# Kernel tuning notes

Measured on AMD Instinct MI355X. Metric: run time of the kernel, lower is better.

## Reference

```python
import jax, jax.numpy as jnp
import numpy as np
import math

JULIA_ITERS = 64
ESCAPE_RADIUS = 2.0


def _julia_escape_times(seq_len, c_real, c_imag):
    # Positions mapped to the real segment [-2, 2]; iterate z <- z^2 + c,
    # record (first iteration index where |z| > R) / ITERS, else 1.0.
    x = jnp.linspace(-2.0, 2.0, seq_len)
    zr0 = x
    zi0 = jnp.zeros_like(x)
    escaped0 = jnp.zeros(seq_len, dtype=bool)
    et0 = jnp.ones(seq_len, dtype=x.dtype)
    r2 = ESCAPE_RADIUS * ESCAPE_RADIUS

    def step(carry, it):
        zr, zi, escaped, et = carry
        nzr = zr * zr - zi * zi + c_real
        nzi = 2.0 * zr * zi + c_imag
        # torch breaks out of the loop once escaped -> freeze z afterwards
        zr = jnp.where(escaped, zr, nzr)
        zi = jnp.where(escaped, zi, nzi)
        mag2 = zr * zr + zi * zi
        newly = jnp.logical_and(~escaped, mag2 > r2)
        et = jnp.where(newly, it.astype(et.dtype) / JULIA_ITERS, et)
        escaped = jnp.logical_or(escaped, newly)
        return (zr, zi, escaped, et), None

    (_, _, _, et), _ = jax.lax.scan(step, (zr0, zi0, escaped0, et0), jnp.arange(JULIA_ITERS))
    return et


def setup_inputs() -> dict:
    key = jax.random.key(0)
    kq, kk, kv = jax.random.split(key, 3)
    B, S, D = 4, 8192, 64
    return {
        "query": jax.random.normal(kq, (B, S, D), dtype=jnp.float32),
        "key": jax.random.normal(kk, (B, S, D), dtype=jnp.float32),
        "value": jax.random.normal(kv, (B, S, D), dtype=jnp.float32),
        "julia_c_real": jnp.float32(-0.7),
        "julia_c_imag": jnp.float32(0.27),
        "escape_scale": jnp.float32(1.0),
    }


def reference(query, key, value, julia_c_real, julia_c_imag, escape_scale):
    B, S, D = key.shape
    et = _julia_escape_times(S, julia_c_real, julia_c_imag)            # [S]
    julia_weights = jnp.exp(et * escape_scale)                          # [S]
    bias = jnp.log(julia_weights + 1e-8)                                # [S]
    scores = jnp.einsum("bqd,bkd->bqk", query, key) / math.sqrt(D)     # [B,S,S]
    scores = scores + bias[None, None, :]
    attn = jax.nn.softmax(scores, axis=-1)
    out = jnp.einsum("bqk,bkd->bqd", attn, value)                       # [B,S,D]
    return out  # squeeze(1) is a no-op for S > 1
```

## Files before the change

### kernel.cpp

```cpp
#include <hip/hip_runtime.h>
#include <math.h>

#define S_LEN 8192
#define DHEAD 64
#define NBATCH 4
#define BK 32
#define KIT 64

typedef unsigned short u16;
typedef unsigned int u32;
typedef __attribute__((ext_vector_type(8))) short short8;
typedef __attribute__((ext_vector_type(4))) float f32x4;

union U16x8 { int4 i4; short8 s8; u32 w[4]; };

#if __has_builtin(__builtin_amdgcn_exp2f)
#define EXP2(x) __builtin_amdgcn_exp2f(x)
#else
#define EXP2(x) exp2f(x)
#endif

__device__ __forceinline__ u16 f2b(float f) {
    u32 u = __float_as_uint(f);
    u32 r = (u + 0x7fffu + ((u >> 16) & 1u)) >> 16;
    return (u16)r;
}

__device__ __forceinline__ u32 pack2(float a, float b) {
    u32 ua = __float_as_uint(a) + 0x8000u;
    u32 ub = __float_as_uint(b) + 0x8000u;
    return __builtin_amdgcn_perm(ub, ua, 0x07060302u);
}

__global__ void prep_kernel(const float* __restrict__ K, const float* __restrict__ V,
                            const float* crp, const float* cip, const float* scp,
                            u16* __restrict__ blob, float* __restrict__ bias2) {
    int bid = blockIdx.x, tid = threadIdx.x;
    if (bid < 1024) {
        int b = bid >> 8, t = bid & 255;
        __shared__ float Kt[32 * 64];
        __shared__ float Vt[32 * 65];
        int row = tid >> 3, c8 = (tid & 7) * 8;
        const float* ks = K + ((size_t)(b * S_LEN + t * 32 + row)) * 64 + c8;
        const float* vs = V + ((size_t)(b * S_LEN + t * 32 + row)) * 64 + c8;
        float4 ka = *(const float4*)ks, kb4 = *(const float4*)(ks + 4);
        float4 va = *(const float4*)vs, vb4 = *(const float4*)(vs + 4);
        *(float4*)&Kt[row * 64 + c8] = ka;
        *(float4*)&Kt[row * 64 + c8 + 4] = kb4;
        float* vr = &Vt[row * 65 + c8];
        vr[0] = va.x; vr[1] = va.y; vr[2] = va.z; vr[3] = va.w;
        vr[4] = vb4.x; vr[5] = vb4.y; vr[6] = vb4.z; vr[7] = vb4.w;
        __syncthreads();

        int j = tid >> 6, lane = tid & 63, low = lane & 15, h = lane >> 4;
        u16* tb = blob + ((size_t)(b * 256 + t)) * 4096;
        {
            int kt = j >> 1, ds = j & 1;
            int krow = 8 * (low >> 2) + 4 * kt + (low & 3);
            const float* src = &Kt[krow * 64 + ds * 32 + h * 8];
            u32 wds[4];
#pragma unroll
            for (int i = 0; i < 4; ++i)
                wds[i] = (u32)f2b(src[2 * i]) | ((u32)f2b(src[2 * i + 1]) << 16);
            *(int4*)(tb + j * 512 + lane * 8) = make_int4(wds[0], wds[1], wds[2], wds[3]);
        }
        {
            int col = j * 16 + low;
            u32 wds[4];
#pragma unroll
            for (int i = 0; i < 4; ++i) {
                float a = Vt[(h * 8 + 2 * i) * 65 + col];
                float c = Vt[(h * 8 + 2 * i + 1) * 65 + col];
                wds[i] = (u32)f2b(a) | ((u32)f2b(c) << 16);
            }
            *(int4*)(tb + 2048 + j * 512 + lane * 8) = make_int4(wds[0], wds[1], wds[2], wds[3]);
        }
    } else {
#pragma clang fp contract(off)
        int i = (bid - 1024) * 256 + tid;
        double cr = (double)crp[0], ci = (double)cip[0], sc = (double)scp[0];
        double step = 4.0 / (double)(S_LEN - 1);
        double x = (i == S_LEN - 1) ? 2.0 : (-2.0 + step * (double)i);
        double zr = x, zi = 0.0, et = 1.0;
        bool esc = false;
        for (int it = 0; it < 64; ++it) {
            double nzr = zr * zr - zi * zi + cr;
            double nzi = 2.0 * zr * zi + ci;
            if (!esc) { zr = nzr; zi = nzi; }
            double m2 = zr * zr + zi * zi;
            if (!esc && m2 > 4.0) { et = (double)it / 64.0; esc = true; }
        }
        double bias = log(exp(et * sc) + 1e-8);
        bias2[i] = (float)(bias * 1.4426950408889634 - 20.0);
    }
}

__global__ __launch_bounds__(512, 4)
void flash_kernel(const float* __restrict__ Q, const u16* __restrict__ blob,
                  const float* __restrict__ bias2, float* __restrict__ Out) {
    __shared__ __align__(16) char smem[18432];

    const int tid = threadIdx.x;
    const int l = tid & 63, low = l & 15, h = l >> 4;
    const int kq = __builtin_amdgcn_readfirstlane((tid >> 6) & 3);
    const int qs = __builtin_amdgcn_readfirstlane(tid >> 8);

    const int bid = blockIdx.x;
    const int batch = bid & 3;
    const int qtile = bid >> 2;
    const int q0 = qtile * 64 + qs * 32;

    const float qscale = 0.18033688011112042f;
    short8 qfrag[2][2];
#pragma unroll
    for (int qf = 0; qf < 2; ++qf) {
        const float* qrow = Q + ((size_t)(batch * S_LEN + q0 + qf * 16 + low)) * DHEAD + h * 8;
#pragma unroll
        for (int ds = 0; ds < 2; ++ds) {
            f32x4 a = *(const f32x4*)(qrow + ds * 32);
            f32x4 b = *(const f32x4*)(qrow + ds * 32 + 4);
            U16x8 u;
#pragma unroll
            for (int jj = 0; jj < 4; ++jj) {
                u.s8[jj]     = (short)f2b(a[jj] * qscale);
                u.s8[4 + jj] = (short)f2b(b[jj] * qscale);
            }
            qfrag[qf][ds] = u.s8;
        }
    }

    const u16* kvb = blob + ((size_t)(batch * 256 + kq * 64)) * 4096;
    const int loff = l * 8;
    const float* bbase = bias2 + kq * 2048;

    f32x4 o[2][4];
#pragma unroll
    for (int qf = 0; qf < 2; ++qf)
#pragma unroll
        for (int dt = 0; dt < 4; ++dt) o[qf][dt] = (f32x4){0, 0, 0, 0};
    float lsum[2] = {0.f, 0.f};

#pragma unroll 1
    for (int ki = 0; ki < KIT; ++ki) {
        const u16* tb = kvb + ki * 4096;
        U16x8 kf[4], vf[4];
#pragma unroll
        for (int j = 0; j < 4; ++j) kf[j].i4 = *(const int4*)(tb + j * 512 + loff);
#pragma unroll
        for (int j = 0; j < 4; ++j) vf[j].i4 = *(const int4*)(tb + 2048 + j * 512 + loff);
        const float* bp = bbase + ki * 32 + h * 8;
        f32x4 bv0 = *(const f32x4*)bp;
        f32x4 bv1 = *(const f32x4*)(bp + 4);

        U16x8 pf[2];
#pragma unroll
        for (int kt = 0; kt < 2; ++kt) {
            const f32x4 binit = kt ? bv1 : bv0;
            f32x4 st[2];
#pragma unroll
            for (int qf = 0; qf < 2; ++qf) {
                f32x4 a = __builtin_amdgcn_mfma_f32_16x16x32_bf16(kf[kt * 2].s8, qfrag[qf][0], binit, 0, 0, 0);
                a = __builtin_amdgcn_mfma_f32_16x16x32_bf16(kf[kt * 2 + 1].s8, qfrag[qf][1], a, 0, 0, 0);
                st[qf] = a;
            }
#pragma unroll
            for (int qf = 0; qf < 2; ++qf) {
                float p0 = EXP2(st[qf][0]), p1 = EXP2(st[qf][1]);
                float p2 = EXP2(st[qf][2]), p3 = EXP2(st[qf][3]);
                lsum[qf] += (p0 + p1) + (p2 + p3);
                pf[qf].w[kt * 2]     = pack2(p0, p1);
                pf[qf].w[kt * 2 + 1] = pack2(p2, p3);
            }
        }

#pragma unroll
        for (int dt = 0; dt < 4; ++dt)
#pragma unroll
            for (int qf = 0; qf < 2; ++qf)
                o[qf][dt] = __builtin_amdgcn_mfma_f32_16x16x32_bf16(vf[dt].s8, pf[qf].s8, o[qf][dt], 0, 0, 0);
    }

#pragma unroll
    for (int qf = 0; qf < 2; ++qf) {
        lsum[qf] += __shfl_xor(lsum[qf], 16, 64);
        lsum[qf] += __shfl_xor(lsum[qf], 32, 64);
    }

    float* MO = (float*)smem;
    float* ML = (float*)(smem + 17408);
    const int baserow = qs * 32 + low;
#pragma unroll 1
    for (int src = 1; src < 4; ++src) {
        __syncthreads();
        if (kq == src) {
#pragma unroll
            for (int qf = 0; qf < 2; ++qf) {
                const int row = baserow + qf * 16;
#pragma unroll
                for (int dt = 0; dt < 4; ++dt)
                    *(f32x4*)&MO[row * 68 + dt * 16 + h * 4] = o[qf][dt];
                if (h == 0) ML[row] = lsum[qf];
            }
        }
        __syncthreads();
        if (kq == 0) {
#pragma unroll
            for (int qf = 0; qf < 2; ++qf) {
                const int row = baserow + qf * 16;
#pragma unroll
                for (int dt = 0; dt < 4; ++dt) {
                    f32x4 a = *(const f32x4*)&MO[row * 68 + dt * 16 + h * 4];
#pragma unroll
                    for (int jj = 0; jj < 4; ++jj) o[qf][dt][jj] += a[jj];
                }
                lsum[qf] += ML[row];
            }
        }
    }

    if (kq == 0) {
#pragma unroll
        for (int qf = 0; qf < 2; ++qf) {
            const float inv = 1.f / lsum[qf];
            float* orow = Out + ((size_t)(batch * S_LEN + qtile * 64 + qs * 32 + qf * 16 + low)) * DHEAD;
#pragma unroll
            for (int dt = 0; dt < 4; ++dt) {
                f32x4 r;
#pragma unroll
                for (int jj = 0; jj < 4; ++jj) r[jj] = o[qf][dt][jj] * inv;
                *(f32x4*)(orow + dt * 16 + h * 4) = r;
            }
        }
    }
}

extern "C" void kernel_launch(void* const* d_in, const int* in_sizes, int n_in,
                              void* d_out, int out_size, void* d_ws, size_t ws_size,
                              hipStream_t stream) {
    const float* Q  = (const float*)d_in[0];
    const float* K  = (const float*)d_in[1];
    const float* V  = (const float*)d_in[2];
    const float* cr = (const float*)d_in[3];
    const float* ci = (const float*)d_in[4];
    const float* sc = (const float*)d_in[5];
    float* out = (float*)d_out;

    char* ws = (char*)d_ws;
    float* bias2 = (float*)ws;
    u16*   blob  = (u16*)(ws + 32768);

    prep_kernel<<<dim3(1056), dim3(256), 0, stream>>>(K, V, cr, ci, sc, blob, bias2);
    flash_kernel<<<dim3(512), dim3(512), 0, stream>>>(Q, blob, bias2, out);
}
```

Baseline: 167.3 us.

## Prefetch next K tile and bias, switch PV matmul to fp16

K fragments and bias values for the next key tile are now loaded one iteration ahead into double-buffered registers, and the loop is unrolled by two. This is meant to hide global load latency behind the current tile's MFMA and exp work. V and the probabilities are now stored and packed as fp16 with a single cvt_pkrtz instruction instead of a manual bf16 rounding, and the PV product uses the f16 MFMA. The prefetch reads one tile past the end on the last iteration, and the change raises register pressure. fp16 narrows the exponent range, so large values could overflow.

```diff
diff --git a/kernel.cpp b/kernel.cpp
--- a/kernel.cpp
+++ b/kernel.cpp
@@ -10,9 +10,14 @@
 typedef unsigned short u16;
 typedef unsigned int u32;
 typedef __attribute__((ext_vector_type(8))) short short8;
+typedef __attribute__((ext_vector_type(8))) _Float16 half8;
+typedef __attribute__((ext_vector_type(2))) __fp16 fp16x2;
 typedef __attribute__((ext_vector_type(4))) float f32x4;
 
 union U16x8 { int4 i4; short8 s8; u32 w[4]; };
+union HU8  { int4 i4; half8 h8; u32 w[4]; };
+union H2U  { fp16x2 h2; u32 w; };
+union HU   { _Float16 h; u16 u; };
 
 #if __has_builtin(__builtin_amdgcn_exp2f)
 #define EXP2(x) __builtin_amdgcn_exp2f(x)
@@ -25,11 +30,11 @@
     u32 r = (u + 0x7fffu + ((u >> 16) & 1u)) >> 16;
     return (u16)r;
 }
-
-__device__ __forceinline__ u32 pack2(float a, float b) {
-    u32 ua = __float_as_uint(a) + 0x8000u;
-    u32 ub = __float_as_uint(b) + 0x8000u;
-    return __builtin_amdgcn_perm(ub, ua, 0x07060302u);
+__device__ __forceinline__ u16 f2h(float f) {
+    HU x; x.h = (_Float16)f; return x.u;
+}
+__device__ __forceinline__ u32 packh2(float a, float b) {
+    H2U x; x.h2 = __builtin_amdgcn_cvt_pkrtz(a, b); return x.w;
 }
 
 __global__ void prep_kernel(const float* __restrict__ K, const float* __restrict__ V,
@@ -71,7 +76,7 @@
             for (int i = 0; i < 4; ++i) {
                 float a = Vt[(h * 8 + 2 * i) * 65 + col];
                 float c = Vt[(h * 8 + 2 * i + 1) * 65 + col];
-                wds[i] = (u32)f2b(a) | ((u32)f2b(c) << 16);
+                wds[i] = (u32)f2h(a) | ((u32)f2h(c) << 16);
             }
             *(int4*)(tb + 2048 + j * 512 + lane * 8) = make_int4(wds[0], wds[1], wds[2], wds[3]);
         }
@@ -140,27 +145,38 @@
         for (int dt = 0; dt < 4; ++dt) o[qf][dt] = (f32x4){0, 0, 0, 0};
     float lsum[2] = {0.f, 0.f};
 
-#pragma unroll 1
+    U16x8 kf[2][4];
+    f32x4 bvv[2][2];
+#pragma unroll
+    for (int j = 0; j < 4; ++j) kf[0][j].i4 = *(const int4*)(kvb + j * 512 + loff);
+    bvv[0][0] = *(const f32x4*)(bbase + h * 8);
+    bvv[0][1] = *(const f32x4*)(bbase + h * 8 + 4);
+
+#pragma unroll 2
     for (int ki = 0; ki < KIT; ++ki) {
+        const int c = ki & 1;
         const u16* tb = kvb + ki * 4096;
-        U16x8 kf[4], vf[4];
-#pragma unroll
-        for (int j = 0; j < 4; ++j) kf[j].i4 = *(const int4*)(tb + j * 512 + loff);
+
+        HU8 vf[4];
 #pragma unroll
         for (int j = 0; j < 4; ++j) vf[j].i4 = *(const int4*)(tb + 2048 + j * 512 + loff);
-        const float* bp = bbase + ki * 32 + h * 8;
-        f32x4 bv0 = *(const f32x4*)bp;
-        f32x4 bv1 = *(const f32x4*)(bp + 4);
-
-        U16x8 pf[2];
+
+        const u16* tn = tb + 4096;
+#pragma unroll
+        for (int j = 0; j < 4; ++j) kf[c ^ 1][j].i4 = *(const int4*)(tn + j * 512 + loff);
+        const float* bpn = bbase + (ki + 1) * 32 + h * 8;
+        bvv[c ^ 1][0] = *(const f32x4*)bpn;
+        bvv[c ^ 1][1] = *(const f32x4*)(bpn + 4);
+
+        HU8 pf[2];
 #pragma unroll
         for (int kt = 0; kt < 2; ++kt) {
-            const f32x4 binit = kt ? bv1 : bv0;
+            const f32x4 binit = kt ? bvv[c][1] : bvv[c][0];
             f32x4 st[2];
 #pragma unroll
             for (int qf = 0; qf < 2; ++qf) {
-                f32x4 a = __builtin_amdgcn_mfma_f32_16x16x32_bf16(kf[kt * 2].s8, qfrag[qf][0], binit, 0, 0, 0);
-                a = __builtin_amdgcn_mfma_f32_16x16x32_bf16(kf[kt * 2 + 1].s8, qfrag[qf][1], a, 0, 0, 0);
+                f32x4 a = __builtin_amdgcn_mfma_f32_16x16x32_bf16(kf[c][kt * 2].s8, qfrag[qf][0], binit, 0, 0, 0);
+                a = __builtin_amdgcn_mfma_f32_16x16x32_bf16(kf[c][kt * 2 + 1].s8, qfrag[qf][1], a, 0, 0, 0);
                 st[qf] = a;
             }
 #pragma unroll
@@ -168,8 +184,8 @@
                 float p0 = EXP2(st[qf][0]), p1 = EXP2(st[qf][1]);
                 float p2 = EXP2(st[qf][2]), p3 = EXP2(st[qf][3]);
                 lsum[qf] += (p0 + p1) + (p2 + p3);
-                pf[qf].w[kt * 2]     = pack2(p0, p1);
-                pf[qf].w[kt * 2 + 1] = pack2(p2, p3);
+                pf[qf].w[kt * 2]     = packh2(p0, p1);
+                pf[qf].w[kt * 2 + 1] = packh2(p2, p3);
             }
         }
 
@@ -177,7 +193,7 @@
         for (int dt = 0; dt < 4; ++dt)
 #pragma unroll
             for (int qf = 0; qf < 2; ++qf)
-                o[qf][dt] = __builtin_amdgcn_mfma_f32_16x16x32_bf16(vf[dt].s8, pf[qf].s8, o[qf][dt], 0, 0, 0);
+                o[qf][dt] = __builtin_amdgcn_mfma_f32_16x16x32_f16(vf[dt].h8, pf[qf].h8, o[qf][dt], 0, 0, 0);
     }
 
 #pragma unroll
```

New measurement: 171.7 us. 2.6% more time.
